# Kernel tuning notes

Measured on AMD Instinct MI355X. Metric: run time of the kernel, lower is better.

Reference implementation:

```python
import jax, jax.numpy as jnp
import numpy as np

D = 512
H = 8
DK = D // H
EXP = 2
EPS = 1e-5


def _layernorm(x, g, b):
    mu = jnp.mean(x, axis=-1, keepdims=True)
    var = jnp.mean(jnp.square(x - mu), axis=-1, keepdims=True)
    return (x - mu) * jax.lax.rsqrt(var + EPS) * g + b


def setup_inputs() -> dict:
    key = jax.random.key(0)
    ks = jax.random.split(key, 10)
    B, C = 4, 2048
    s = 0.02
    return {
        "h": jax.random.normal(ks[0], (B, C, D), jnp.float32),
        "adj_bias": jax.random.normal(ks[1], (B, C, C), jnp.float32),
        "w_qkv": jax.random.normal(ks[2], (D, 3 * D), jnp.float32) * s,
        "b_qkv": jnp.zeros((3 * D,), jnp.float32),
        "w_out": jax.random.normal(ks[3], (D, D), jnp.float32) * s,
        "b_out": jnp.zeros((D,), jnp.float32),
        "ln1_g": jnp.ones((D,), jnp.float32),
        "ln1_b": jnp.zeros((D,), jnp.float32),
        "ln2_g": jnp.ones((D,), jnp.float32),
        "ln2_b": jnp.zeros((D,), jnp.float32),
        "w1": jax.random.normal(ks[4], (D, D * EXP), jnp.float32) * s,
        "b1": jnp.zeros((D * EXP,), jnp.float32),
        "w2": jax.random.normal(ks[5], (D * EXP, D), jnp.float32) * s,
        "b2": jnp.zeros((D,), jnp.float32),
    }


def reference(h, adj_bias, w_qkv, b_qkv, w_out, b_out, ln1_g, ln1_b, ln2_g, ln2_b, w1, b1, w2, b2):
    B, C, _ = h.shape
    scale = DK ** -0.5
    h_n = _layernorm(h, ln1_g, ln1_b)
    qkv = (h_n @ w_qkv + b_qkv).reshape(B, C, 3, H, DK)
    q, k, v = (qkv[:, :, i].transpose(0, 2, 1, 3) for i in range(3))  # (B,H,C,DK)
    logits = jnp.einsum('bhqd,bhkd->bhqk', q, k) * scale + adj_bias[:, None, :, :]
    attn = jax.nn.softmax(logits, axis=-1)  # (B,H,C,C); dropout off (eval)
    out = jnp.einsum('bhqk,bhkd->bhqd', attn, v).transpose(0, 2, 1, 3).reshape(B, C, D)
    h = h + out @ w_out + b_out
    ff = _layernorm(h, ln2_g, ln2_b)
    ff = jax.nn.gelu(ff @ w1 + b1, approximate=False) @ w2 + b2
    return h + ff
```

## Files before the change

kernel.cpp:

```cpp
#include <hip/hip_runtime.h>
#include <hip/hip_bf16.h>

#define BDIM 4
#define CDIM 2048
#define DDIM 512
#define HH   8
#define DKH  64
#define NROW (BDIM * CDIM)

typedef unsigned short u16;
typedef unsigned int   u32;
typedef u16   u16x4  __attribute__((ext_vector_type(4)));
typedef u16   u16x8  __attribute__((ext_vector_type(8)));
typedef u32   u32x4  __attribute__((ext_vector_type(4)));
typedef __bf16 bf16x8 __attribute__((ext_vector_type(8)));
typedef __bf16 bf16x2 __attribute__((ext_vector_type(2)));
typedef float f32x4  __attribute__((ext_vector_type(4)));
typedef float f32x16 __attribute__((ext_vector_type(16)));

#define LOG2E 1.4426950408889634f

#define MEMFENCE asm volatile("" ::: "memory")
__device__ __forceinline__ void sbar() {
  MEMFENCE; __builtin_amdgcn_s_barrier(); MEMFENCE;
}
#define VMWAIT(N) asm volatile("s_waitcnt vmcnt(" #N ")" ::: "memory")

__device__ __forceinline__ u16 f2bf(float f) {
  union { float f; unsigned u; } x; x.f = f;
  unsigned u = x.u;
  u += 0x7fffu + ((u >> 16) & 1u);
  return (u16)(u >> 16);
}
__device__ __forceinline__ float bf2f(u16 u) {
  return __builtin_bit_cast(float, (u32)u << 16);
}
__device__ __forceinline__ u32 pk2(float a, float b) {
  bf16x2 t; t[0] = (__bf16)a; t[1] = (__bf16)b;
  return __builtin_bit_cast(u32, t);
}
__device__ __forceinline__ float fexp2(float x) {
  float r;
  asm("v_exp_f32 %0, %1" : "=v"(r) : "v"(x));
  return r;
}

__device__ __forceinline__ void gload_lds16(const u16* gp, u16* lp) {
  __builtin_amdgcn_global_load_lds((__attribute__((address_space(1))) const void*)gp,
                                   (__attribute__((address_space(3))) void*)lp, 16, 0, 0);
}

__device__ __forceinline__ void ln_body(int bx, int tid,
                                        const float* __restrict__ x,
                                        const float* __restrict__ gamma,
                                        const float* __restrict__ beta,
                                        u16* __restrict__ y) {
  int gw = (bx * 256 + tid) >> 6;
  int l  = tid & 63;
  const float* xr = x + (size_t)gw * DDIM;
  float4 a = *(const float4*)(xr + l * 8);
  float4 b = *(const float4*)(xr + l * 8 + 4);
  float s = a.x + a.y + a.z + a.w + b.x + b.y + b.z + b.w;
  float q = a.x*a.x + a.y*a.y + a.z*a.z + a.w*a.w + b.x*b.x + b.y*b.y + b.z*b.z + b.w*b.w;
#pragma unroll
  for (int m = 1; m < 64; m <<= 1) { s += __shfl_xor(s, m); q += __shfl_xor(q, m); }
  float mu  = s * (1.0f / DDIM);
  float var = q * (1.0f / DDIM) - mu * mu;
  float rs  = rsqrtf(var + 1e-5f);
  float4 g0 = *(const float4*)(gamma + l * 8);
  float4 g1 = *(const float4*)(gamma + l * 8 + 4);
  float4 b0 = *(const float4*)(beta + l * 8);
  float4 b1 = *(const float4*)(beta + l * 8 + 4);
  u16x8 o;
  o[0] = f2bf((a.x - mu) * rs * g0.x + b0.x);
  o[1] = f2bf((a.y - mu) * rs * g0.y + b0.y);
  o[2] = f2bf((a.z - mu) * rs * g0.z + b0.z);
  o[3] = f2bf((a.w - mu) * rs * g0.w + b0.w);
  o[4] = f2bf((b.x - mu) * rs * g1.x + b1.x);
  o[5] = f2bf((b.y - mu) * rs * g1.y + b1.y);
  o[6] = f2bf((b.z - mu) * rs * g1.z + b1.z);
  o[7] = f2bf((b.w - mu) * rs * g1.w + b1.w);
  *(u16x8*)(y + (size_t)gw * DDIM + l * 8) = o;
}

__global__ __launch_bounds__(256) void ln_kernel(const float* __restrict__ x,
                                                 const float* __restrict__ gamma,
                                                 const float* __restrict__ beta,
                                                 u16* __restrict__ y) {
  ln_body(blockIdx.x, threadIdx.x, x, gamma, beta, y);
}

__device__ __forceinline__ void adj_body(int f, int t,
                                         const float* __restrict__ adj,
                                         u16* __restrict__ adjC) {
  const int b = f >> 8, kt = (f >> 3) & 31;
  const int q0 = (f & 7) * 256;
  const int ch = t & 7, c16 = ch & 3, hi2 = ch >> 2, m = c16 >> 1;
  const int K0 = m * 32 + ((c16 * 2) & 3) * 8 + hi2 * 4;
#pragma unroll
  for (int itq = 0; itq < 8; ++itq) {
    int q = q0 + itq * 32 + (t >> 3);
    const float* src = adj + ((size_t)b * CDIM + q) * CDIM + kt * 64;
    f32x4 v0 = *(const f32x4*)(src + K0);
    f32x4 v1 = *(const f32x4*)(src + K0 + 8);
    u16x8 o;
    o[0] = f2bf(v0[0] * LOG2E); o[1] = f2bf(v0[1] * LOG2E);
    o[2] = f2bf(v0[2] * LOG2E); o[3] = f2bf(v0[3] * LOG2E);
    o[4] = f2bf(v1[0] * LOG2E); o[5] = f2bf(v1[1] * LOG2E);
    o[6] = f2bf(v1[2] * LOG2E); o[7] = f2bf(v1[3] * LOG2E);
    *(u16x8*)(adjC + ((size_t)(b * 32 + kt) * 2048 + q) * 64 + ch * 8) = o;
  }
}

__global__ __launch_bounds__(256) void setup_kernel(const float* __restrict__ h,
                                                    const float* __restrict__ ln1g,
                                                    const float* __restrict__ ln1b,
                                                    u16* __restrict__ hn,
                                                    const float* __restrict__ wqkv,
                                                    const float* __restrict__ wout,
                                                    const float* __restrict__ w1,
                                                    const float* __restrict__ w2,
                                                    u16* __restrict__ o_qkv,
                                                    u16* __restrict__ o_out,
                                                    u16* __restrict__ o_w1,
                                                    u16* __restrict__ o_w2) {
  const int bx = blockIdx.x;
  const int t = threadIdx.x;
  if (bx < 2048) {
    ln_body(bx, t, h, ln1g, ln1b, hn);
  } else {
    int idx = (bx - 2048) * 256 + t;
    const float* w; u16* wt; int K, N;
    if (idx < 98304)       { w = wqkv; wt = o_qkv; K = 512;  N = 1536; }
    else if (idx < 131072) { idx -= 98304;  w = wout; wt = o_out; K = 512;  N = 512; }
    else if (idx < 196608) { idx -= 131072; w = w1;   wt = o_w1;  K = 512;  N = 1024; }
    else                   { idx -= 196608; w = w2;   wt = o_w2;  K = 1024; N = 512; }
    int kb = K >> 3;
    int n = idx / kb, k0 = (idx - n * kb) * 8;
    u16x8 o;
#pragma unroll
    for (int j = 0; j < 8; ++j) o[j] = f2bf(w[(size_t)(k0 + j) * N + n]);
    *(u16x8*)(wt + (size_t)n * K + k0) = o;
  }
}

template <int EPI>
__device__ __forceinline__ void gemm_epi(int row, int col, float val, int N,
                                         const float* __restrict__ res,
                                         float* __restrict__ outf,
                                         u16* __restrict__ outb,
                                         u16* __restrict__ outq,
                                         u16* __restrict__ outk,
                                         u16* __restrict__ outv) {
  if constexpr (EPI == 0) {
    int t = col >> 9, hh = (col >> 6) & 7, dk = col & 63;
    int bb = row >> 11, cc = row & 2047;
    if (t == 0) {
      val *= 0.125f * LOG2E;
      outq[(((size_t)bb * HH + hh) * CDIM + cc) * DKH + dk] = f2bf(val);
    } else if (t == 1) {
      outk[(((size_t)bb * HH + hh) * CDIM + cc) * DKH + dk] = f2bf(val);
    } else {
      outv[(((size_t)bb * HH + hh) * DKH + dk) * CDIM + cc] = f2bf(val);
    }
  } else if constexpr (EPI == 1) {
    size_t idx = (size_t)row * N + col;
    outf[idx] = val + res[idx];
  } else {
    float g = 0.5f * val * (1.0f + erff(val * 0.70710678118f));
    outb[(size_t)row * N + col] = f2bf(g);
  }
}

template <int EPI>
__device__ __forceinline__ void gemm128_body(int flat, int nbn, int nwg,
                                             const u16* __restrict__ A,
                                             const u16* __restrict__ Bt,
                                             const float* __restrict__ bias,
                                             const float* __restrict__ res,
                                             float* __restrict__ outf,
                                             u16* __restrict__ outb,
                                             u16* __restrict__ outq,
                                             u16* __restrict__ outk,
                                             u16* __restrict__ outv,
                                             int N, int K) {
  __shared__ u16 As[3][128 * 32];
  __shared__ u16 Bs[3][128 * 32];
  const int tid = threadIdx.x;
  const int w = tid >> 6, l = tid & 63;
  const int l15 = l & 15, l4 = l >> 4;
  const int virt = (flat & 7) * (nwg >> 3) + (flat >> 3);
  const int bn = virt % nbn, bm = virt / nbn;
  const int wr = w >> 1, wc = w & 1;

  f32x4 acc[4][4] = {};

  const int sg = (l & 3) ^ ((l >> 2) & 3);
  const u16* Ag = A  + (size_t)(bm * 128 + w * 32 + (l >> 2)) * K + sg * 8;
  const u16* Bg = Bt + (size_t)(bn * 128 + w * 32 + (l >> 2)) * K + sg * 8;

  auto stage = [&](int buf, int k0) {
    gload_lds16(Ag + k0,                  &As[buf][(w * 32 + 0) * 32]);
    gload_lds16(Ag + (size_t)16 * K + k0, &As[buf][(w * 32 + 16) * 32]);
    gload_lds16(Bg + k0,                  &Bs[buf][(w * 32 + 0) * 32]);
    gload_lds16(Bg + (size_t)16 * K + k0, &Bs[buf][(w * 32 + 16) * 32]);
  };

  const int nk = K >> 5;
  stage(0, 0);
  int bcur = 0, bnxt = 1;
#pragma unroll 1
  for (int i = 0; i < nk; ++i) {
    if (i + 1 < nk) {
      stage(bnxt, (i + 1) * 32);
      VMWAIT(4);
    } else {
      VMWAIT(0);
    }
    sbar();
    const u16* AsC = &As[bcur][0];
    const u16* BsC = &Bs[bcur][0];
    bf16x8 af[4], bf[4];
#pragma unroll
    for (int m = 0; m < 4; ++m)
      af[m] = *(const bf16x8*)(&AsC[(wr * 64 + m * 16 + l15) * 32 + ((l4 ^ (l15 & 3)) * 8)]);
#pragma unroll
    for (int n = 0; n < 4; ++n)
      bf[n] = *(const bf16x8*)(&BsC[(wc * 64 + n * 16 + l15) * 32 + ((l4 ^ (l15 & 3)) * 8)]);
#pragma unroll
    for (int m = 0; m < 4; ++m)
#pragma unroll
      for (int n = 0; n < 4; ++n)
        acc[m][n] = __builtin_amdgcn_mfma_f32_16x16x32_bf16(af[m], bf[n], acc[m][n], 0, 0, 0);
    bcur = bnxt;
    bnxt = bnxt + 1 == 3 ? 0 : bnxt + 1;
  }

#pragma unroll
  for (int m = 0; m < 4; ++m) {
    const int row0 = bm * 128 + wr * 64 + m * 16 + l4 * 4;
#pragma unroll
    for (int n = 0; n < 4; ++n) {
      const int col = bn * 128 + wc * 64 + n * 16 + l15;
      const float bv = bias[col];
#pragma unroll
      for (int r = 0; r < 4; ++r)
        gemm_epi<EPI>(row0 + r, col, acc[m][n][r] + bv, N, res, outf, outb, outq, outk, outv);
    }
  }
}

__global__ __launch_bounds__(256) void qkv_adj_kernel(const u16* __restrict__ A,
                                                      const u16* __restrict__ Bt,
                                                      const float* __restrict__ bias,
                                                      u16* __restrict__ outq,
                                                      u16* __restrict__ outk,
                                                      u16* __restrict__ outv,
                                                      const float* __restrict__ adj,
                                                      u16* __restrict__ adjC) {
  if (blockIdx.x < 768) {
    gemm128_body<0>(blockIdx.x, 12, 768, A, Bt, bias, nullptr,
                    nullptr, nullptr, outq, outk, outv, 3 * DDIM, DDIM);
  } else {
    adj_body(blockIdx.x - 768, threadIdx.x, adj, adjC);
  }
}

template <int EPI>
__global__ __launch_bounds__(256) void gemm128k(const u16* __restrict__ A,
                                                const u16* __restrict__ Bt,
                                                const float* __restrict__ bias,
                                                const float* __restrict__ res,
                                                float* __restrict__ outf,
                                                u16* __restrict__ outb,
                                                int M, int N, int K) {
  gemm128_body<EPI>(blockIdx.x + gridDim.x * blockIdx.y, gridDim.x,
                    gridDim.x * gridDim.y, A, Bt, bias, res,
                    outf, outb, nullptr, nullptr, nullptr, N, K);
}

template <int EPI>
__global__ __launch_bounds__(256) void gemm64(const u16* __restrict__ A,
                                              const u16* __restrict__ Bt,
                                              const float* __restrict__ bias,
                                              const float* __restrict__ res,
                                              float* __restrict__ outf,
                                              u16* __restrict__ outb,
                                              int M, int N, int K) {
  __shared__ u16 As[2][64 * 64];
  __shared__ u16 Bs[2][128 * 64];
  const int tid = threadIdx.x;
  const int w = tid >> 6, l = tid & 63;
  const int l15 = l & 15, l4 = l >> 4, l7 = l15 & 7;
  const int nbn = gridDim.x, nwg = gridDim.x * gridDim.y;
  const int flat = blockIdx.x + nbn * blockIdx.y;
  const int virt = (flat & 7) * (nwg >> 3) + (flat >> 3);
  const int bn = virt % nbn, bm = virt / nbn;

  f32x4 acc[4][2] = {};

  const int sg = (l & 7) ^ (l >> 3);
  const u16* Ag = A  + (size_t)(bm * 64  + w * 16 + (l >> 3)) * K + sg * 8;
  const u16* Bg = Bt + (size_t)(bn * 128 + w * 32 + (l >> 3)) * K + sg * 8;

  auto stage = [&](int buf, int k0) {
    gload_lds16(Ag + k0,                  &As[buf][(w * 16 + 0) * 64]);
    gload_lds16(Ag + (size_t)8 * K + k0,  &As[buf][(w * 16 + 8) * 64]);
    gload_lds16(Bg + k0,                  &Bs[buf][(w * 32 + 0) * 64]);
    gload_lds16(Bg + (size_t)8 * K + k0,  &Bs[buf][(w * 32 + 8) * 64]);
    gload_lds16(Bg + (size_t)16 * K + k0, &Bs[buf][(w * 32 + 16) * 64]);
    gload_lds16(Bg + (size_t)24 * K + k0, &Bs[buf][(w * 32 + 24) * 64]);
  };

  stage(0, 0);
  __syncthreads();
  int cur = 0;
  for (int k0 = 0; k0 < K; k0 += 64) {
    if (k0 + 64 < K) stage(cur ^ 1, k0 + 64);
#pragma unroll
    for (int s = 0; s < 2; ++s) {
      bf16x8 af[4], bf[2];
#pragma unroll
      for (int m = 0; m < 4; ++m)
        af[m] = *(const bf16x8*)(&As[cur][(m * 16 + l15) * 64 + (((s * 4 + l4) ^ l7) * 8)]);
#pragma unroll
      for (int n = 0; n < 2; ++n)
        bf[n] = *(const bf16x8*)(&Bs[cur][(w * 32 + n * 16 + l15) * 64 + (((s * 4 + l4) ^ l7) * 8)]);
#pragma unroll
      for (int m = 0; m < 4; ++m)
#pragma unroll
        for (int n = 0; n < 2; ++n)
          acc[m][n] = __builtin_amdgcn_mfma_f32_16x16x32_bf16(af[m], bf[n], acc[m][n], 0, 0, 0);
    }
    __syncthreads();
    cur ^= 1;
  }

#pragma unroll
  for (int m = 0; m < 4; ++m) {
    const int row0 = bm * 64 + m * 16 + l4 * 4;
#pragma unroll
    for (int n = 0; n < 2; ++n) {
      const int col = bn * 128 + w * 32 + n * 16 + l15;
      const float bv = bias[col];
#pragma unroll
      for (int r = 0; r < 4; ++r)
        gemm_epi<EPI>(row0 + r, col, acc[m][n][r] + bv, N, res, outf, outb,
                      nullptr, nullptr, nullptr);
    }
  }
}

__global__ __launch_bounds__(512, 2) void flash_attn(const u16* __restrict__ Q,
                                                     const u16* __restrict__ Kg,
                                                     const u16* __restrict__ Vt,
                                                     const u16* __restrict__ adjC,
                                                     u16* __restrict__ O) {
  __shared__ u16 Ks[2][2][64 * 64];
  __shared__ u16 Vs[2][2][64 * 64];
  __shared__ float lw[4][32];
  __shared__ float lsx[4][32];
  const int flat = blockIdx.x + 16 * blockIdx.y;
  const int virt = (flat & 7) * 64 + (flat >> 3);
  const int qt = virt & 15;
  const int bh = virt >> 4;
  const int b = bh >> 3, hh = bh & 7;
  const int tid = threadIdx.x;
  const int w = tid >> 6, l = tid & 63;
  const int kh = w >> 2, qg = w & 3;
  const int q32 = l & 31, hi = l >> 5;
  const int qglob = qt * 128 + qg * 32 + q32;

  const u16* Qb = Q  + (size_t)bh * CDIM * DKH;
  const u16* Kb = Kg + (size_t)bh * CDIM * DKH;
  const u16* Vb = Vt + (size_t)bh * DKH * CDIM;

  const int srow = qg * 16 + (l >> 3);
  const int sg   = (l & 7) ^ (l >> 3);
  const u16* Kg0 = Kb + (size_t)(srow + 0) * DKH + sg * 8;
  const u16* Kg1 = Kb + (size_t)(srow + 8) * DKH + sg * 8;
  const u16* Vg0 = Vb + (size_t)(srow + 0) * CDIM + sg * 8;
  const u16* Vg1 = Vb + (size_t)(srow + 8) * CDIM + sg * 8;

  bf16x8 qf[4];
#pragma unroll
  for (int s = 0; s < 4; ++s)
    qf[s] = *(const bf16x8*)(Qb + (size_t)qglob * DKH + s * 16 + hi * 8);

  const u16* adjQ = adjC + ((size_t)(b * 32) * 2048 + qglob) * 64 + hi * 32;

  f32x16 oa[2] = {};
  float lsum = 0.f;

  auto stage = [&](int buf, int ktr) {
    int kta = kh * 16 + ktr;
    gload_lds16(Kg0 + (size_t)kta * 4096, &Ks[kh][buf][(qg * 16 + 0) * 64]);
    gload_lds16(Kg1 + (size_t)kta * 4096, &Ks[kh][buf][(qg * 16 + 8) * 64]);
    gload_lds16(Vg0 + kta * 64, &Vs[kh][buf][(qg * 16 + 0) * 64]);
    gload_lds16(Vg1 + kta * 64, &Vs[kh][buf][(qg * 16 + 8) * 64]);
  };
  auto ajload = [&](u16x8* dst, int ktr) {
    const u16* p = adjQ + (size_t)(kh * 16 + ktr) * 131072;
#pragma unroll
    for (int i = 0; i < 4; ++i) dst[i] = *(const u16x8*)(p + i * 8);
  };
  auto computeQK = [&](const u16* KsB, const u16x8* av, f32x16* sa) {
#pragma unroll
    for (int m = 0; m < 2; ++m)
#pragma unroll
      for (int r = 0; r < 16; ++r)
        sa[m][r] = bf2f(av[m * 2 + (r >> 3)][r & 7]);
    __builtin_amdgcn_s_setprio(1);
#pragma unroll
    for (int s = 0; s < 4; ++s)
#pragma unroll
      for (int m = 0; m < 2; ++m) {
        bf16x8 kf = *(const bf16x8*)(&KsB[(m * 32 + q32) * 64 + (((s * 2 + hi) ^ (q32 & 7)) * 8)]);
        sa[m] = __builtin_amdgcn_mfma_f32_32x32x16_bf16(kf, qf[s], sa[m], 0, 0, 0);
      }
    __builtin_amdgcn_s_setprio(0);
  };
  auto computePV = [&](const u16* VsB, f32x16* sa) {
#pragma unroll
    for (int m = 0; m < 2; ++m)
#pragma unroll
      for (int r = 0; r < 16; ++r) {
        float p = fexp2(sa[m][r]);
        sa[m][r] = p;
        lsum += p;
      }
    bf16x8 af[4];
#pragma unroll
    for (int m = 0; m < 2; ++m)
#pragma unroll
      for (int t2 = 0; t2 < 2; ++t2) {
        u32 w0 = pk2(sa[m][t2 * 8 + 0], sa[m][t2 * 8 + 1]);
        u32 w1 = pk2(sa[m][t2 * 8 + 2], sa[m][t2 * 8 + 3]);
        u32 w2 = pk2(sa[m][t2 * 8 + 4], sa[m][t2 * 8 + 5]);
        u32 w3 = pk2(sa[m][t2 * 8 + 6], sa[m][t2 * 8 + 7]);
        auto r02 = __builtin_amdgcn_permlane32_swap(w0, w2, false, false);
        auto r13 = __builtin_amdgcn_permlane32_swap(w1, w3, false, false);
        u32x4 aw;
        aw[0] = r02[0];
        aw[1] = r13[0];
        aw[2] = r02[1];
        aw[3] = r13[1];
        af[m * 2 + t2] = __builtin_bit_cast(bf16x8, aw);
      }
    __builtin_amdgcn_s_setprio(1);
#pragma unroll
    for (int s = 0; s < 4; ++s)
#pragma unroll
      for (int n = 0; n < 2; ++n) {
        bf16x8 vf = *(const bf16x8*)(&VsB[(n * 32 + q32) * 64 + (((s * 2 + hi) ^ (q32 & 7)) * 8)]);
        oa[n] = __builtin_amdgcn_mfma_f32_32x32x16_bf16(af[s], vf, oa[n], 0, 0, 0);
      }
    __builtin_amdgcn_s_setprio(0);
  };

  u16x8 avA[4], avB[4];
  f32x16 sa[2];
  stage(0, 0);
  ajload(avA, 0);
  __syncthreads();
#pragma unroll 1
  for (int it = 0; it < 8; ++it) {
    int ktr = it * 2;
    stage(1, ktr + 1);
    computeQK(&Ks[kh][0][0], avA, sa);
    ajload(avB, ktr + 1);
    computePV(&Vs[kh][0][0], sa);
    __syncthreads();
    if (ktr + 2 < 16) stage(0, ktr + 2);
    computeQK(&Ks[kh][1][0], avB, sa);
    if (ktr + 2 < 16) ajload(avA, ktr + 2);
    computePV(&Vs[kh][1][0], sa);
    __syncthreads();
  }

  lsum += __shfl_xor(lsum, 32);

  float* cb = (float*)&Vs[0][0][0];
  if (kh == 1) {
#pragma unroll
    for (int n = 0; n < 2; ++n)
#pragma unroll
      for (int r = 0; r < 16; ++r)
        cb[((qg * 2 + n) * 16 + r) * 64 + l] = oa[n][r];
    if (hi == 0) lsx[qg][q32] = lsum;
  }
  __syncthreads();
  if (kh == 0) {
    lsum += lsx[qg][q32];
#pragma unroll
    for (int n = 0; n < 2; ++n)
#pragma unroll
      for (int r = 0; r < 16; ++r)
        oa[n][r] += cb[((qg * 2 + n) * 16 + r) * 64 + l];
    lw[qg][q32] = 1.0f / lsum;
#pragma unroll
    for (int n = 0; n < 2; ++n)
#pragma unroll
      for (int r = 0; r < 16; ++r) {
        int qloc = (r & 3) + 8 * (r >> 2) + 4 * hi;
        int row = qt * 128 + qg * 32 + qloc;
        float val = oa[n][r] * lw[qg][qloc];
        O[((size_t)b * CDIM + row) * DDIM + hh * 64 + n * 32 + q32] = f2bf(val);
      }
  }
}

extern "C" void kernel_launch(void* const* d_in, const int* in_sizes, int n_in,
                              void* d_out, int out_size, void* d_ws, size_t ws_size,
                              hipStream_t stream) {
  const float* h      = (const float*)d_in[0];
  const float* adj    = (const float*)d_in[1];
  const float* w_qkv  = (const float*)d_in[2];
  const float* b_qkv  = (const float*)d_in[3];
  const float* w_out  = (const float*)d_in[4];
  const float* b_out  = (const float*)d_in[5];
  const float* ln1g   = (const float*)d_in[6];
  const float* ln1b   = (const float*)d_in[7];
  const float* ln2g   = (const float*)d_in[8];
  const float* ln2b   = (const float*)d_in[9];
  const float* w1     = (const float*)d_in[10];
  const float* b1     = (const float*)d_in[11];
  const float* w2     = (const float*)d_in[12];
  const float* b2     = (const float*)d_in[13];
  float* out = (float*)d_out;

  char* ws = (char*)d_ws;
  u16* adjC  = (u16*)(ws);
  u16* hn    = (u16*)(ws + 33554432);
  u16* qb    = (u16*)(ws + 41943040);
  u16* kb    = (u16*)(ws + 50331648);
  u16* vt    = (u16*)(ws + 58720256);
  u16* attn  = (u16*)(ws + 67108864);
  u16* wqkvt = (u16*)(ws + 75497472);
  u16* woutt = (u16*)(ws + 77070336);
  u16* w1t   = (u16*)(ws + 77594624);
  u16* w2t   = (u16*)(ws + 78643200);
  u16* ffin  = hn;
  u16* ffmid = qb;

  setup_kernel<<<3072, 256, 0, stream>>>(h, ln1g, ln1b, hn,
                                         w_qkv, w_out, w1, w2,
                                         wqkvt, woutt, w1t, w2t);

  qkv_adj_kernel<<<1792, 256, 0, stream>>>(hn, wqkvt, b_qkv, qb, kb, vt,
                                           adj, adjC);

  flash_attn<<<dim3(16, 32), 512, 0, stream>>>(qb, kb, vt, adjC, attn);

  gemm64<1><<<dim3(4, 128), 256, 0, stream>>>(attn, woutt, b_out, h,
                                              out, nullptr, NROW, DDIM, DDIM);

  ln_kernel<<<2048, 256, 0, stream>>>(out, ln2g, ln2b, ffin);

  gemm128k<2><<<dim3(8, 64), 256, 0, stream>>>(ffin, w1t, b1, nullptr,
                                               nullptr, ffmid, NROW, 2 * DDIM, DDIM);

  gemm64<1><<<dim3(4, 128), 256, 0, stream>>>(ffmid, w2t, b2, out,
                                              out, nullptr, NROW, DDIM, 2 * DDIM);
}
```

Before: 176.7 us.

## Use triple-buffered K=32 staging with single barrier in gemm64

```diff
diff --git a/kernel.cpp b/kernel.cpp
--- a/kernel.cpp
+++ b/kernel.cpp
@@ -287,11 +287,11 @@
                                               float* __restrict__ outf,
                                               u16* __restrict__ outb,
                                               int M, int N, int K) {
-  __shared__ u16 As[2][64 * 64];
-  __shared__ u16 Bs[2][128 * 64];
+  __shared__ u16 As[3][64 * 32];
+  __shared__ u16 Bs[3][128 * 32];
   const int tid = threadIdx.x;
   const int w = tid >> 6, l = tid & 63;
-  const int l15 = l & 15, l4 = l >> 4, l7 = l15 & 7;
+  const int l15 = l & 15, l4 = l >> 4;
   const int nbn = gridDim.x, nwg = gridDim.x * gridDim.y;
   const int flat = blockIdx.x + nbn * blockIdx.y;
   const int virt = (flat & 7) * (nwg >> 3) + (flat >> 3);
@@ -299,41 +299,44 @@
 
   f32x4 acc[4][2] = {};
 
-  const int sg = (l & 7) ^ (l >> 3);
-  const u16* Ag = A  + (size_t)(bm * 64  + w * 16 + (l >> 3)) * K + sg * 8;
-  const u16* Bg = Bt + (size_t)(bn * 128 + w * 32 + (l >> 3)) * K + sg * 8;
+  const int sg = (l & 3) ^ ((l >> 2) & 3);
+  const u16* Ag = A  + (size_t)(bm * 64  + w * 16 + (l >> 2)) * K + sg * 8;
+  const u16* Bg = Bt + (size_t)(bn * 128 + w * 32 + (l >> 2)) * K + sg * 8;
 
   auto stage = [&](int buf, int k0) {
-    gload_lds16(Ag + k0,                  &As[buf][(w * 16 + 0) * 64]);
-    gload_lds16(Ag + (size_t)8 * K + k0,  &As[buf][(w * 16 + 8) * 64]);
-    gload_lds16(Bg + k0,                  &Bs[buf][(w * 32 + 0) * 64]);
-    gload_lds16(Bg + (size_t)8 * K + k0,  &Bs[buf][(w * 32 + 8) * 64]);
-    gload_lds16(Bg + (size_t)16 * K + k0, &Bs[buf][(w * 32 + 16) * 64]);
-    gload_lds16(Bg + (size_t)24 * K + k0, &Bs[buf][(w * 32 + 24) * 64]);
+    gload_lds16(Ag + k0,                  &As[buf][(w * 16) * 32]);
+    gload_lds16(Bg + k0,                  &Bs[buf][(w * 32 + 0) * 32]);
+    gload_lds16(Bg + (size_t)16 * K + k0, &Bs[buf][(w * 32 + 16) * 32]);
   };
 
+  const int nk = K >> 5;
   stage(0, 0);
-  __syncthreads();
-  int cur = 0;
-  for (int k0 = 0; k0 < K; k0 += 64) {
-    if (k0 + 64 < K) stage(cur ^ 1, k0 + 64);
-#pragma unroll
-    for (int s = 0; s < 2; ++s) {
-      bf16x8 af[4], bf[2];
-#pragma unroll
-      for (int m = 0; m < 4; ++m)
-        af[m] = *(const bf16x8*)(&As[cur][(m * 16 + l15) * 64 + (((s * 4 + l4) ^ l7) * 8)]);
+  int bcur = 0, bnxt = 1;
+#pragma unroll 1
+  for (int i = 0; i < nk; ++i) {
+    if (i + 1 < nk) {
+      stage(bnxt, (i + 1) * 32);
+      VMWAIT(3);
+    } else {
+      VMWAIT(0);
+    }
+    sbar();
+    const u16* AsC = &As[bcur][0];
+    const u16* BsC = &Bs[bcur][0];
+    bf16x8 af[4], bf[2];
+#pragma unroll
+    for (int m = 0; m < 4; ++m)
+      af[m] = *(const bf16x8*)(&AsC[(m * 16 + l15) * 32 + ((l4 ^ (l15 & 3)) * 8)]);
+#pragma unroll
+    for (int n = 0; n < 2; ++n)
+      bf[n] = *(const bf16x8*)(&BsC[(w * 32 + n * 16 + l15) * 32 + ((l4 ^ (l15 & 3)) * 8)]);
+#pragma unroll
+    for (int m = 0; m < 4; ++m)
 #pragma unroll
       for (int n = 0; n < 2; ++n)
-        bf[n] = *(const bf16x8*)(&Bs[cur][(w * 32 + n * 16 + l15) * 64 + (((s * 4 + l4) ^ l7) * 8)]);
-#pragma unroll
-      for (int m = 0; m < 4; ++m)
-#pragma unroll
-        for (int n = 0; n < 2; ++n)
-          acc[m][n] = __builtin_amdgcn_mfma_f32_16x16x32_bf16(af[m], bf[n], acc[m][n], 0, 0, 0);
-    }
-    __syncthreads();
-    cur ^= 1;
+        acc[m][n] = __builtin_amdgcn_mfma_f32_16x16x32_bf16(af[m], bf[n], acc[m][n], 0, 0, 0);
+    bcur = bnxt;
+    bnxt = bnxt + 1 == 3 ? 0 : bnxt + 1;
   }
 
 #pragma unroll
```

New measurement: 178.2 us. About the same (+0.9%).
